# Kernel tuning notes

Hardware: AMD Instinct MI355X
Metric: run time of the kernel (lower is better)

The kernel has to match this reference:

```python
import jax, jax.numpy as jnp
import numpy as np

STEEPNESS = 10.0
EPS = 1e-12

def _l2norm(x):
    return x / jnp.sqrt(jnp.sum(x * x, axis=-1, keepdims=True) + EPS)

def setup_inputs() -> dict:
    key = jax.random.key(0)
    k1, k2, k3 = jax.random.split(key, 3)
    B, D, C = 65536, 512, 1024
    return {
        "query": jax.random.normal(k1, (B, D), dtype=jnp.float32),
        "key_mem": jax.random.normal(k2, (C, D), dtype=jnp.float32),
        "val_mem": jax.random.normal(k3, (C, C), dtype=jnp.float32),
    }

def reference(query, key_mem, val_mem):
    # F.normalize(query_vectors, dim=-1)
    q = _l2norm(query)                      # (B, D)
    # cosine_similarity_multi(q, key_mem, rep='real'):
    # F.linear(F.normalize(a), F.normalize(b)) -> (B, C)
    k = _l2norm(key_mem)                    # (C, D)
    sim = jnp.einsum('bd,cd->bc', q, k)     # (B, C)
    # softabs sharpening: sigmoid(s*(x-0.5)) + sigmoid(s*(-x-0.5))
    s = STEEPNESS
    sharp = jax.nn.sigmoid(s * sim - 0.5 * s) + jax.nn.sigmoid(-s * sim - 0.5 * s)
    # normalize_weightings
    w = sharp / jnp.sum(sharp, axis=1, keepdims=True)
    # weighted value readout
    out = jnp.matmul(w, val_mem)            # (B, C)
    return out
```

## Files before the change

kernel.cpp:

```cpp
#include <hip/hip_runtime.h>
#include <hip/hip_bf16.h>

typedef __attribute__((ext_vector_type(8))) short bf16x8;
typedef __attribute__((ext_vector_type(8))) unsigned short ushort8;
typedef __attribute__((ext_vector_type(4))) float f32x4;
typedef unsigned int u32;

#define D_DIM 512
#define C_DIM 1024

__device__ __forceinline__ unsigned short f2bf(float x) {
  u32 u = __float_as_uint(x);
  u32 r = (u + 0x7fffu + ((u >> 16) & 1u)) >> 16;
  return (unsigned short)r;
}

__device__ __forceinline__ void async16(const void* g, void* l) {
  __builtin_amdgcn_global_load_lds(
      (const __attribute__((address_space(1))) u32*)g,
      (__attribute__((address_space(3))) u32*)l, 16, 0, 0);
}

__global__ __launch_bounds__(256) void rownorm_kernel(
    const float* __restrict__ src, unsigned short* __restrict__ dst) {
  int row = blockIdx.x * 4 + (threadIdx.x >> 6);
  int lane = threadIdx.x & 63;
  const float* s = src + (size_t)row * D_DIM + lane * 8;
  float4 v0 = *(const float4*)s;
  float4 v1 = *(const float4*)(s + 4);
  float ss = v0.x * v0.x + v0.y * v0.y + v0.z * v0.z + v0.w * v0.w +
             v1.x * v1.x + v1.y * v1.y + v1.z * v1.z + v1.w * v1.w;
#pragma unroll
  for (int m = 32; m >= 1; m >>= 1) ss += __shfl_xor(ss, m);
  float rinv = rsqrtf(ss + 1e-12f);
  float tv[8] = {v0.x, v0.y, v0.z, v0.w, v1.x, v1.y, v1.z, v1.w};
  ushort8 o;
#pragma unroll
  for (int i = 0; i < 8; ++i) o[i] = f2bf(tv[i] * rinv);
  *(ushort8*)(dst + (size_t)row * D_DIM + lane * 8) = o;
}

__global__ __launch_bounds__(256) void valT_kernel(
    const float* __restrict__ val, unsigned short* __restrict__ vbT) {
  __shared__ float tile[32][33];
  int bx = blockIdx.x & 31;
  int by = blockIdx.x >> 5;
  int t = threadIdx.x;
  int r = t >> 5, c = t & 31;
#pragma unroll
  for (int i = 0; i < 4; ++i)
    tile[r + i * 8][c] = val[(size_t)(by * 32 + r + i * 8) * C_DIM + bx * 32 + c];
  __syncthreads();
#pragma unroll
  for (int i = 0; i < 4; ++i)
    vbT[(size_t)(bx * 32 + r + i * 8) * C_DIM + by * 32 + c] = f2bf(tile[c][r + i * 8]);
}

template <int K, bool SHARP>
__global__ __launch_bounds__(512, 2) void gemm256_kernel(
    const unsigned short* __restrict__ A, const unsigned short* __restrict__ Bm,
    unsigned short* __restrict__ wout, float* __restrict__ rsum,
    float* __restrict__ fout) {
  __shared__ unsigned short smem[65536];
  const int NKT = K / 64;
  const int bid = blockIdx.x;
  const int wg = (bid & 7) * 128 + (bid >> 3);
  const int m0 = (wg >> 2) * 256;
  const int n0 = (wg & 3) * 256;
  const int t = threadIdx.x;
  const int lane = t & 63;
  const int wv = t >> 6;
  const int wr = wv >> 2;
  const int wc = wv & 3;
  const int lo = lane & 15, hi = lane >> 4;
  const int swu = (lo & 7) << 3;

  const int s_ridx = t >> 3;
  const int s_c = (t & 7) * 8;
  auto stage = [&](int T, int k) {
    int r = (s_ridx < 32) ? (k * 32 + s_ridx) : (96 + k * 32 + s_ridx);
    int cl = s_c ^ ((r & 7) << 3);
    size_t go = (size_t)T * 64 + cl;
    int d = (T & 1) * 32768;
    async16(A + (size_t)(m0 + r) * K + go, &smem[d + r * 64 + s_c]);
    async16(Bm + (size_t)(n0 + r) * K + go, &smem[d + 16384 + r * 64 + s_c]);
  };

  f32x4 acc[8][4];
#pragma unroll
  for (int i = 0; i < 8; ++i)
#pragma unroll
    for (int j = 0; j < 4; ++j) acc[i][j] = (f32x4){0.f, 0.f, 0.f, 0.f};

  stage(0, 0); stage(0, 1); stage(0, 2); stage(0, 3);
  stage(1, 0); stage(1, 1); stage(1, 2);

#pragma unroll 1
  for (int T = 0; T < NKT; ++T) {
    if (T == NKT - 1) {
      asm volatile("s_waitcnt vmcnt(0)" ::: "memory");
    } else {
      asm volatile("s_waitcnt vmcnt(6)" ::: "memory");
    }
    __builtin_amdgcn_s_barrier();
    const int d = (T & 1) * 32768;
    bf16x8 bfr[4][2];
#pragma unroll
    for (int p = 0; p < 4; ++p) {
      bf16x8 af[2][2];
#pragma unroll
      for (int mi = 0; mi < 2; ++mi)
#pragma unroll
        for (int ks = 0; ks < 2; ++ks) {
          int r = wr * 128 + (p * 2 + mi) * 16 + lo;
          af[mi][ks] = *(const bf16x8*)&smem[d + r * 64 + ((ks * 32 + hi * 8) ^ swu)];
        }
      if (p == 0) {
#pragma unroll
        for (int nf = 0; nf < 4; ++nf)
#pragma unroll
          for (int ks = 0; ks < 2; ++ks) {
            int r = wc * 64 + nf * 16 + lo;
            bfr[nf][ks] =
                *(const bf16x8*)&smem[d + 16384 + r * 64 + ((ks * 32 + hi * 8) ^ swu)];
          }
        if (T + 1 < NKT) stage(T + 1, 3);
      } else {
        if (T + 2 < NKT) stage(T + 2, p - 1);
      }
      __builtin_amdgcn_s_barrier();
      __builtin_amdgcn_s_setprio(1);
#pragma unroll
      for (int mi = 0; mi < 2; ++mi)
#pragma unroll
        for (int nf = 0; nf < 4; ++nf)
#pragma unroll
          for (int ks = 0; ks < 2; ++ks)
            acc[p * 2 + mi][nf] = __builtin_amdgcn_mfma_f32_16x16x32_bf16(
                af[mi][ks], bfr[nf][ks], acc[p * 2 + mi][nf], 0, 0, 0);
      __builtin_amdgcn_s_setprio(0);
      __builtin_amdgcn_s_barrier();
    }
  }
  __syncthreads();

  if (SHARP) {
    float rs[8][4];
#pragma unroll
    for (int i = 0; i < 8; ++i)
#pragma unroll
      for (int j = 0; j < 4; ++j) rs[i][j] = 0.f;
    unsigned short* ep = smem;
#pragma unroll
    for (int mf = 0; mf < 8; ++mf)
#pragma unroll
      for (int nf = 0; nf < 4; ++nf)
#pragma unroll
        for (int j = 0; j < 4; ++j) {
          float x = acc[mf][nf][j];
          float s = 1.f / (1.f + __expf(5.f - 10.f * x)) +
                    1.f / (1.f + __expf(5.f + 10.f * x));
          rs[mf][j] += s;
          int rl = wr * 128 + mf * 16 + (hi << 2) + j;
          int cl = wc * 64 + nf * 16 + lo;
          ep[rl * 256 + cl] = f2bf(s);
        }
#pragma unroll
    for (int mf = 0; mf < 8; ++mf)
#pragma unroll
      for (int j = 0; j < 4; ++j) {
        float v = rs[mf][j];
        v += __shfl_xor(v, 1);
        v += __shfl_xor(v, 2);
        v += __shfl_xor(v, 4);
        v += __shfl_xor(v, 8);
        if (lo == 0)
          atomicAdd(&rsum[m0 + wr * 128 + mf * 16 + (hi << 2) + j], v);
      }
    __syncthreads();
#pragma unroll
    for (int pass = 0; pass < 16; ++pass) {
      int idx = pass * 4096 + t * 8;
      int row = idx >> 8, col = idx & 255;
      *(ushort8*)&wout[(size_t)(m0 + row) * C_DIM + n0 + col] = *(const ushort8*)&ep[idx];
    }
  } else {
    float rinv[8][4];
#pragma unroll
    for (int mf = 0; mf < 8; ++mf)
#pragma unroll
      for (int j = 0; j < 4; ++j)
        rinv[mf][j] = 1.f / rsum[m0 + wr * 128 + mf * 16 + (hi << 2) + j];
#pragma unroll
    for (int mf = 0; mf < 8; ++mf)
#pragma unroll
      for (int nf = 0; nf < 4; ++nf)
#pragma unroll
        for (int j = 0; j < 4; ++j)
          fout[(size_t)(m0 + wr * 128 + mf * 16 + (hi << 2) + j) * C_DIM +
               n0 + wc * 64 + nf * 16 + lo] = acc[mf][nf][j] * rinv[mf][j];
  }
}

extern "C" void kernel_launch(void* const* d_in, const int* in_sizes, int n_in,
                              void* d_out, int out_size, void* d_ws, size_t ws_size,
                              hipStream_t stream) {
  const float* query = (const float*)d_in[0];
  const float* key = (const float*)d_in[1];
  const float* val = (const float*)d_in[2];
  float* out = (float*)d_out;
  const int B = in_sizes[0] / D_DIM;

  char* ws = (char*)d_ws;
  unsigned short* kb = (unsigned short*)(ws);
  unsigned short* vbT = (unsigned short*)(ws + (1ull << 20));
  float* rsum = (float*)(ws + 3ull * (1ull << 20));
  unsigned short* qb = (unsigned short*)(ws + 4ull * (1ull << 20));
  unsigned short* wbf = (unsigned short*)(ws + 68ull * (1ull << 20));

  rownorm_kernel<<<dim3(B / 4), dim3(256), 0, stream>>>(query, qb);
  rownorm_kernel<<<dim3(C_DIM / 4), dim3(256), 0, stream>>>(key, kb);
  valT_kernel<<<dim3(1024), dim3(256), 0, stream>>>(val, vbT);
  hipMemsetAsync(rsum, 0, (size_t)B * sizeof(float), stream);

  dim3 grid((B / 256) * (C_DIM / 256));
  gemm256_kernel<D_DIM, true><<<grid, dim3(512), 0, stream>>>(qb, kb, wbf, rsum, nullptr);
  gemm256_kernel<C_DIM, false><<<grid, dim3(512), 0, stream>>>(wbf, vbT, nullptr, rsum, out);
}
```

Before: 381.4 us.

## Trim per-phase barriers in GEMM main loop and use fast sigmoid/rcp math

Peels phase 0 of the K-loop out on its own so it runs without the pre-MFMA barrier, and drops the trailing barrier after each MFMA phase. In phases 1-3 the async stage issue now comes after the remaining barrier, so fewer workgroup syncs separate LDS reads, prefetches and MFMAs. The softabs epilogue now takes one exp plus hardware reciprocals instead of two exps and two divides, and the final row normalisation uses rcp. The risks are a race where a prefetch overwrites an LDS buffer another wave is still reading, and small accuracy loss from approximate reciprocals.

```diff
diff --git a/kernel.cpp b/kernel.cpp
--- a/kernel.cpp
+++ b/kernel.cpp
@@ -19,6 +19,12 @@
   __builtin_amdgcn_global_load_lds(
       (const __attribute__((address_space(1))) u32*)g,
       (__attribute__((address_space(3))) u32*)l, 16, 0, 0);
+}
+
+__device__ __forceinline__ float sharpf(float x) {
+  float t = __expf(10.f * x - 5.f);
+  return t * __builtin_amdgcn_rcpf(1.f + t) +
+         __builtin_amdgcn_rcpf(1.f + t * 22026.4658f);
 }
 
 __global__ __launch_bounds__(256) void rownorm_kernel(
@@ -105,8 +111,37 @@
     __builtin_amdgcn_s_barrier();
     const int d = (T & 1) * 32768;
     bf16x8 bfr[4][2];
-#pragma unroll
-    for (int p = 0; p < 4; ++p) {
+    {
+      bf16x8 af[2][2];
+#pragma unroll
+      for (int mi = 0; mi < 2; ++mi)
+#pragma unroll
+        for (int ks = 0; ks < 2; ++ks) {
+          int r = wr * 128 + mi * 16 + lo;
+          af[mi][ks] = *(const bf16x8*)&smem[d + r * 64 + ((ks * 32 + hi * 8) ^ swu)];
+        }
+#pragma unroll
+      for (int nf = 0; nf < 4; ++nf)
+#pragma unroll
+        for (int ks = 0; ks < 2; ++ks) {
+          int r = wc * 64 + nf * 16 + lo;
+          bfr[nf][ks] =
+              *(const bf16x8*)&smem[d + 16384 + r * 64 + ((ks * 32 + hi * 8) ^ swu)];
+        }
+      if (T + 1 < NKT) stage(T + 1, 3);
+      __builtin_amdgcn_s_setprio(1);
+#pragma unroll
+      for (int mi = 0; mi < 2; ++mi)
+#pragma unroll
+        for (int nf = 0; nf < 4; ++nf)
+#pragma unroll
+          for (int ks = 0; ks < 2; ++ks)
+            acc[mi][nf] = __builtin_amdgcn_mfma_f32_16x16x32_bf16(
+                af[mi][ks], bfr[nf][ks], acc[mi][nf], 0, 0, 0);
+      __builtin_amdgcn_s_setprio(0);
+    }
+#pragma unroll
+    for (int p = 1; p < 4; ++p) {
       bf16x8 af[2][2];
 #pragma unroll
       for (int mi = 0; mi < 2; ++mi)
@@ -115,20 +150,8 @@
           int r = wr * 128 + (p * 2 + mi) * 16 + lo;
           af[mi][ks] = *(const bf16x8*)&smem[d + r * 64 + ((ks * 32 + hi * 8) ^ swu)];
         }
-      if (p == 0) {
-#pragma unroll
-        for (int nf = 0; nf < 4; ++nf)
-#pragma unroll
-          for (int ks = 0; ks < 2; ++ks) {
-            int r = wc * 64 + nf * 16 + lo;
-            bfr[nf][ks] =
-                *(const bf16x8*)&smem[d + 16384 + r * 64 + ((ks * 32 + hi * 8) ^ swu)];
-          }
-        if (T + 1 < NKT) stage(T + 1, 3);
-      } else {
-        if (T + 2 < NKT) stage(T + 2, p - 1);
-      }
       __builtin_amdgcn_s_barrier();
+      if (T + 2 < NKT) stage(T + 2, p - 1);
       __builtin_amdgcn_s_setprio(1);
 #pragma unroll
       for (int mi = 0; mi < 2; ++mi)
@@ -139,7 +162,6 @@
             acc[p * 2 + mi][nf] = __builtin_amdgcn_mfma_f32_16x16x32_bf16(
                 af[mi][ks], bfr[nf][ks], acc[p * 2 + mi][nf], 0, 0, 0);
       __builtin_amdgcn_s_setprio(0);
-      __builtin_amdgcn_s_barrier();
     }
   }
   __syncthreads();
@@ -157,9 +179,7 @@
       for (int nf = 0; nf < 4; ++nf)
 #pragma unroll
         for (int j = 0; j < 4; ++j) {
-          float x = acc[mf][nf][j];
-          float s = 1.f / (1.f + __expf(5.f - 10.f * x)) +
-                    1.f / (1.f + __expf(5.f + 10.f * x));
+          float s = sharpf(acc[mf][nf][j]);
           rs[mf][j] += s;
           int rl = wr * 128 + mf * 16 + (hi << 2) + j;
           int cl = wc * 64 + nf * 16 + lo;
@@ -190,7 +210,8 @@
     for (int mf = 0; mf < 8; ++mf)
 #pragma unroll
       for (int j = 0; j < 4; ++j)
-        rinv[mf][j] = 1.f / rsum[m0 + wr * 128 + mf * 16 + (hi << 2) + j];
+        rinv[mf][j] =
+            __builtin_amdgcn_rcpf(rsum[m0 + wr * 128 + mf * 16 + (hi << 2) + j]);
 #pragma unroll
     for (int mf = 0; mf < 8; ++mf)
 #pragma unroll
```

Result: faster. 359.6 us (-5.7%).
